# Performance work log

Hardware: AMD Instinct MI355X
Metric: run time of the kernel (lower is better)

Reference implementation:

```python
import jax, jax.numpy as jnp
import numpy as np

B, L, H = 8, 64, 128


def setup_inputs() -> dict:
    key = jax.random.key(0)
    ks = jax.random.split(key, 9)
    s = 1.0 / np.sqrt(H)

    def lin(k, shape):
        return jax.random.uniform(k, shape, jnp.float32, -s, s)

    return {
        "words_feats": jax.random.normal(ks[0], (B, L, H), jnp.float32),
        "words_masks": jnp.ones((B, L), jnp.int32),
        "Wl": lin(ks[1], (H, 1)), "bl": lin(ks[2], (1,)),
        "Wr": lin(ks[3], (H, 1)), "br": lin(ks[4], (1,)),
        "Wrep": lin(ks[5], (H, H)), "brep": lin(ks[6], (H,)),
        "Ws": lin(ks[7], (H, 1)), "bs": lin(ks[8], (1,)),
    }


def reference(words_feats, words_masks, Wl, bl, Wr, br, Wrep, brep, Ws, bs):
    # CYK chart DP. All sentences have full length L (masks all ones), so the
    # chart recursion runs L-1 levels with static trip count.
    Bsz, Ln, Hd = words_feats.shape
    ks_ = jnp.arange(Ln)  # split point k
    js_ = jnp.arange(Ln)  # start position j

    # chart T[b, i, j] = feature of span starting at j with length i+1
    T0 = jnp.zeros((Bsz, Ln, Ln, Hd), words_feats.dtype).at[:, 0].set(words_feats)

    def body(T, i):
        # left child:  T[b, k, j]            -> [B, k, j, H]
        left = T
        # right child: T[b, i-k-1, j+k+1]    -> [B, k, j, H] (clipped; masked below)
        rows = jnp.clip(i - ks_ - 1, 0, Ln - 1)                       # [k]
        cols = jnp.clip(js_[None, :] + ks_[:, None] + 1, 0, Ln - 1)   # [k, j]
        right = T[:, rows[:, None], cols]                             # [B, k, j, H]

        # 2-way attention combine of (left, right)
        sl = left @ Wl + bl                                            # [B, k, j, 1]
        sr = right @ Wr + br
        w = jax.nn.softmax(jnp.concatenate([sl, sr], axis=-1), axis=-1)
        h_hat = w[..., :1] * left + w[..., 1:] * right                 # [B, k, j, H]
        temp = jax.nn.relu(h_hat @ Wrep + brep) + h_hat

        # only k < i splits and spans with i + j < L exist; others are exact
        # zeros (matching the torch zero-initialized temp_h table)
        valid = (ks_[:, None] < i) & (js_[None, :] + i < Ln)           # [k, j]
        temp = jnp.where(valid[None, :, :, None], temp, 0.0)

        # softmax over ALL L split rows (zero rows contribute bias logits,
        # exactly as in the torch code)
        logits = (temp @ Ws + bs)[..., 0]                              # [B, k, j]
        split = jax.nn.softmax(logits, axis=1)                         # over k
        new_row = jnp.einsum('bkj,bkjh->bjh', split, temp)             # [B, j, H]
        new_row = jnp.where((js_ + i < Ln)[None, :, None], new_row, 0.0)
        return T.at[:, i].set(new_row), None

    T, _ = jax.lax.scan(body, T0, jnp.arange(1, Ln))
    return T[:, Ln - 1, 0]  # sentence feature: full span starting at 0
```

## Files before the change

kernel.cpp:

```cpp
#include <hip/hip_runtime.h>
#include <math.h>

#define Hd 128
#define Ln 64
#define Bsz 8
#define NBLK 256
#define NTHR 512
#define SLOTS 32


typedef __attribute__((ext_vector_type(8))) short short8v;
typedef __attribute__((ext_vector_type(4))) float f32x4;

__global__ void init_kernel(const float* __restrict__ wf, float* __restrict__ T,
                            int* __restrict__ flg) {
    int idx = blockIdx.x * 256 + threadIdx.x;
    int b = idx >> 13;
    int rest = idx & 8191;
    T[(size_t)b * (Ln * Ln * Hd) + rest] = wf[idx];
    if (idx < Bsz * Ln * Ln) flg[idx] = 0;
}

__device__ __forceinline__ float2 ld_row8(const float* p) {
    unsigned long long v = __hip_atomic_load((const unsigned long long*)p,
                                             __ATOMIC_RELAXED, __HIP_MEMORY_SCOPE_AGENT);
    return __builtin_bit_cast(float2, v);
}

__device__ __forceinline__ void wait_flag(const int* p) {
    while (__hip_atomic_load(p, __ATOMIC_RELAXED, __HIP_MEMORY_SCOPE_AGENT) == 0)
        __builtin_amdgcn_s_sleep(1);
    asm volatile("" ::: "memory");
}

__device__ __forceinline__ void bf_split3(float x, unsigned short& a0,
                                          unsigned short& a1, unsigned short& a2) {
    unsigned u0 = __builtin_bit_cast(unsigned, x);
    a0 = (unsigned short)(u0 >> 16);
    float f0 = __builtin_bit_cast(float, u0 & 0xffff0000u);
    float r1 = x - f0;
    unsigned u1 = __builtin_bit_cast(unsigned, r1);
    a1 = (unsigned short)(u1 >> 16);
    float f1 = __builtin_bit_cast(float, u1 & 0xffff0000u);
    float r2 = r1 - f1;
    a2 = (unsigned short)(__builtin_bit_cast(unsigned, r2) >> 16);
}

__device__ __forceinline__ float bfval(unsigned short v) {
    return __builtin_bit_cast(float, ((unsigned)v) << 16);
}

#define KSTEP(SK, B0, B1, B2)                                                   \
    {                                                                           \
        int off = ((16 * ch + (ln & 15)) << 7) +                                \
                  ((((SK << 2) + (ln >> 4)) ^ (ln & 15)) << 3);                 \
        short8v a0 = *(const short8v*)&sH0[off];                                \
        short8v a1 = *(const short8v*)&sH1[off];                                \
        short8v a2 = *(const short8v*)&sH2[off];                                \
        acc = __builtin_amdgcn_mfma_f32_16x16x32_bf16(a0, B0, acc, 0, 0, 0);    \
        acc = __builtin_amdgcn_mfma_f32_16x16x32_bf16(a0, B1, acc, 0, 0, 0);    \
        acc = __builtin_amdgcn_mfma_f32_16x16x32_bf16(a1, B0, acc, 0, 0, 0);    \
        acc = __builtin_amdgcn_mfma_f32_16x16x32_bf16(a0, B2, acc, 0, 0, 0);    \
        acc = __builtin_amdgcn_mfma_f32_16x16x32_bf16(a1, B1, acc, 0, 0, 0);    \
        acc = __builtin_amdgcn_mfma_f32_16x16x32_bf16(a2, B0, acc, 0, 0, 0);    \
    }

template<int NCH>
__device__ __forceinline__ void do_cell(
    int i, int jj, int b, int wv, int ln, int tid,
    const float* __restrict__ Tb, float* __restrict__ T, float* __restrict__ out,
    int* __restrict__ flgb,
    unsigned short* __restrict__ sH0, unsigned short* __restrict__ sH1,
    unsigned short* __restrict__ sH2,
    float (*part)[Ln], float* __restrict__ sER,
    const short8v (&B0)[4], const short8v (&B1)[4], const short8v (&B2)[4],
    float2 wlv, float2 wrv, float bl, float br, float bs, float wsc, float bbc)
{
    if (i >= 2) {
        wait_flag(&flgb[(i - 1) * Ln + jj]);
        wait_flag(&flgb[(i - 1) * Ln + jj + 1]);
    }

    float2 Lr[8], Rr[8];
    #pragma unroll
    for (int r = 0; r < 8; ++r) {
        int k = wv + 8 * r;
        int kcl = k < i ? k : i - 1;
        Lr[r] = ld_row8(Tb + ((size_t)kcl * Ln + jj) * Hd + 2 * ln);
        Rr[r] = ld_row8(Tb + ((size_t)(i - 1 - kcl) * Ln + (jj + kcl + 1)) * Hd + 2 * ln);
    }
    float pl[8], pr[8];
    #pragma unroll
    for (int r = 0; r < 8; ++r) {
        pl[r] = Lr[r].x * wlv.x + Lr[r].y * wlv.y;
        pr[r] = Rr[r].x * wrv.x + Rr[r].y * wrv.y;
    }
    #pragma unroll
    for (int off2 = 32; off2 > 0; off2 >>= 1) {
        #pragma unroll
        for (int r = 0; r < 8; ++r) {
            pl[r] += __shfl_xor(pl[r], off2);
            pr[r] += __shfl_xor(pr[r], off2);
        }
    }
    #pragma unroll
    for (int r = 0; r < 8; ++r) {
        int k = wv + 8 * r;
        float sl = pl[r] + bl, sr2 = pr[r] + br;
        float mm = fmaxf(sl, sr2);
        float e0 = __expf(sl - mm), e1 = __expf(sr2 - mm);
        float inv = 1.f / (e0 + e1);
        float w0 = e0 * inv, w1 = e1 * inv;
        float h0 = w0 * Lr[r].x + w1 * Rr[r].x;
        float h1 = w0 * Lr[r].y + w1 * Rr[r].y;
        unsigned short x0, x1, x2, y0, y1, y2;
        bf_split3(h0, x0, x1, x2);
        bf_split3(h1, y0, y1, y2);
        int off = (k << 7) + ((((ln >> 2)) ^ (k & 15)) << 3) + ((2 * ln) & 7);
        *(unsigned*)&sH0[off] = (unsigned)x0 | ((unsigned)y0 << 16);
        *(unsigned*)&sH1[off] = (unsigned)x1 | ((unsigned)y1 << 16);
        *(unsigned*)&sH2[off] = (unsigned)x2 | ((unsigned)y2 << 16);
    }
    __syncthreads();

    const int colc = 16 * wv + (ln & 15);
    float tmp[NCH][4];
    #pragma unroll
    for (int ch = 0; ch < NCH; ++ch) {
        f32x4 acc = {0.f, 0.f, 0.f, 0.f};
        KSTEP(0, B0[0], B1[0], B2[0])
        KSTEP(1, B0[1], B1[1], B2[1])
        KSTEP(2, B0[2], B1[2], B2[2])
        KSTEP(3, B0[3], B1[3], B2[3])
        float p[4];
        #pragma unroll
        for (int q = 0; q < 4; ++q) {
            int row = 16 * ch + (ln >> 4) * 4 + q;
            int offh = (row << 7) + (((colc >> 3) ^ (row & 15)) << 3) + (colc & 7);
            float h = (bfval(sH0[offh]) + bfval(sH1[offh])) + bfval(sH2[offh]);
            float t = fmaxf(acc[q] + bbc, 0.f) + h;
            tmp[ch][q] = t;
            p[q] = t * wsc;
        }
        #pragma unroll
        for (int off2 = 1; off2 <= 8; off2 <<= 1) {
            #pragma unroll
            for (int q = 0; q < 4; ++q) p[q] += __shfl_xor(p[q], off2);
        }
        if ((ln & 15) == 0) {
            #pragma unroll
            for (int q = 0; q < 4; ++q)
                part[wv][16 * ch + (ln >> 4) * 4 + q] = p[q];
        }
    }
    __syncthreads();

    if (wv == 0) {
        float lgv = -INFINITY;
        if (ln < i) {
            float ssum = part[0][ln];
            #pragma unroll
            for (int w = 1; w < 8; ++w) ssum += part[w][ln];
            lgv = ssum + bs;
        }
        float M = lgv;
        #pragma unroll
        for (int off2 = 32; off2 > 0; off2 >>= 1) M = fmaxf(M, __shfl_xor(M, off2));
        M = fmaxf(M, bs);
        float e = (ln < i) ? __expf(lgv - M) : 0.f;
        float S = e;
        #pragma unroll
        for (int off2 = 32; off2 > 0; off2 >>= 1) S += __shfl_xor(S, off2);
        sER[ln] = e;
        if (ln == 0) sER[64] = S + (float)(Ln - i) * __expf(bs - M);
    }
    __syncthreads();

    float v = 0.f;
    #pragma unroll
    for (int ch = 0; ch < NCH; ++ch) {
        #pragma unroll
        for (int q = 0; q < 4; ++q)
            v += sER[16 * ch + (ln >> 4) * 4 + q] * tmp[ch][q];
    }
    v += __shfl_xor(v, 16);
    v += __shfl_xor(v, 32);
    if (ln < 16) {
        float res = v / sER[64];
        __hip_atomic_store(&T[(((size_t)b * Ln + i) * Ln + jj) * Hd + colc], res,
                           __ATOMIC_RELAXED, __HIP_MEMORY_SCOPE_AGENT);
        if (i == Ln - 1) out[b * Hd + colc] = res;
    }
    __syncthreads();
    if (tid == 0)
        __hip_atomic_store(&flgb[i * Ln + jj], 1, __ATOMIC_RELAXED,
                           __HIP_MEMORY_SCOPE_AGENT);
}

__global__ __launch_bounds__(NTHR, 2)
void glt_df(const float* __restrict__ Wl, const float* __restrict__ blp,
            const float* __restrict__ Wr, const float* __restrict__ brp,
            const float* __restrict__ Wrep, const float* __restrict__ brepp,
            const float* __restrict__ Wsv, const float* __restrict__ bsp,
            float* __restrict__ T, int* __restrict__ flg, float* __restrict__ out)
{
    __shared__ __align__(16) unsigned short sH0[Ln * Hd];
    __shared__ __align__(16) unsigned short sH1[Ln * Hd];
    __shared__ __align__(16) unsigned short sH2[Ln * Hd];
    __shared__ float part[8][Ln];
    __shared__ float sER[68];

    const int tid = threadIdx.x;
    const int wv  = tid >> 6;
    const int ln  = tid & 63;
    const int b   = blockIdx.x & 7;
    const int s   = blockIdx.x >> 3;

    const int bcol = 16 * wv + (ln & 15);
    short8v B0[4], B1[4], B2[4];
    #pragma unroll
    for (int sk = 0; sk < 4; ++sk) {
        #pragma unroll
        for (int jx = 0; jx < 8; ++jx) {
            int k = 32 * sk + (ln >> 4) * 8 + jx;
            float w = Wrep[k * Hd + bcol];
            unsigned short w0, w1, w2;
            bf_split3(w, w0, w1, w2);
            B0[sk][jx] = (short)w0;
            B1[sk][jx] = (short)w1;
            B2[sk][jx] = (short)w2;
        }
    }

    const float bl = blp[0], br = brp[0], bs = bsp[0];
    const float2 wlv = *(const float2*)&Wl[2 * ln];
    const float2 wrv = *(const float2*)&Wr[2 * ln];
    const float wsc = Wsv[bcol];
    const float bbc = brepp[bcol];

    const float* Tb = T + (size_t)b * (Ln * Ln * Hd);
    int* flgb = flg + b * (Ln * Ln);

    int i = 1, jj = s;
    while (jj >= Ln - i) { jj -= Ln - i; ++i; }
    for (int t = 0; t < 63; ++t) {
        switch ((i + 15) >> 4) {
            case 1: do_cell<1>(i, jj, b, wv, ln, tid, Tb, T, out, flgb,
                               sH0, sH1, sH2, part, sER, B0, B1, B2,
                               wlv, wrv, bl, br, bs, wsc, bbc); break;
            case 2: do_cell<2>(i, jj, b, wv, ln, tid, Tb, T, out, flgb,
                               sH0, sH1, sH2, part, sER, B0, B1, B2,
                               wlv, wrv, bl, br, bs, wsc, bbc); break;
            case 3: do_cell<3>(i, jj, b, wv, ln, tid, Tb, T, out, flgb,
                               sH0, sH1, sH2, part, sER, B0, B1, B2,
                               wlv, wrv, bl, br, bs, wsc, bbc); break;
            default: do_cell<4>(i, jj, b, wv, ln, tid, Tb, T, out, flgb,
                                sH0, sH1, sH2, part, sER, B0, B1, B2,
                                wlv, wrv, bl, br, bs, wsc, bbc); break;
        }
        if (t < 62) {
            jj += SLOTS;
            while (jj >= Ln - i) { jj -= Ln - i; ++i; }
        }
    }
}

extern "C" void kernel_launch(void* const* d_in, const int* in_sizes, int n_in,
                              void* d_out, int out_size, void* d_ws, size_t ws_size,
                              hipStream_t stream)
{
    const float* wf   = (const float*)d_in[0];
    const float* Wl   = (const float*)d_in[2];
    const float* bl   = (const float*)d_in[3];
    const float* Wr   = (const float*)d_in[4];
    const float* br   = (const float*)d_in[5];
    const float* Wrep = (const float*)d_in[6];
    const float* brep = (const float*)d_in[7];
    const float* Ws   = (const float*)d_in[8];
    const float* bs   = (const float*)d_in[9];

    float* T   = (float*)d_ws;
    int*   flg = (int*)((char*)d_ws + (size_t)Bsz * Ln * Ln * Hd * 4);
    float* out = (float*)d_out;

    init_kernel<<<256, 256, 0, stream>>>(wf, T, flg);

    void* args[] = {(void*)&Wl, (void*)&bl, (void*)&Wr, (void*)&br,
                    (void*)&Wrep, (void*)&brep, (void*)&Ws, (void*)&bs,
                    (void*)&T, (void*)&flg, (void*)&out};
    hipLaunchCooperativeKernel((void*)glt_df, dim3(NBLK), dim3(NTHR),
                               args, 0, stream);
}
```

Measured before the change: 597.7 us.

## Speculatively compute middle splits early, finishing edge splits in fp32 after dependency

Each chart cell now waits only on row i-2 to compute the middle split points k=1..i-2 with MFMA. The two edge splits (k=0 and k=i-1), which depend on row i-1, are computed afterwards by waves 0 and 1 with an fp32 matvec against an LDS copy of Wrep, then merged into the split softmax. This shortens the per-level critical path of the inter-block dataflow wavefront. The cost is 64KB of extra LDS, which likely limits each CU to one block, plus some extra serial work on two waves.

Result: slower. 651.4 us (+9.0%).

```diff
diff --git a/kernel.cpp b/kernel.cpp
--- a/kernel.cpp
+++ b/kernel.cpp
@@ -50,20 +50,69 @@
     return __builtin_bit_cast(float, ((unsigned)v) << 16);
 }
 
-#define KSTEP(SK, B0, B1, B2)                                                   \
+#define KSTEP(SK, B0_, B1_, B2_)                                                \
     {                                                                           \
         int off = ((16 * ch + (ln & 15)) << 7) +                                \
                   ((((SK << 2) + (ln >> 4)) ^ (ln & 15)) << 3);                 \
         short8v a0 = *(const short8v*)&sH0[off];                                \
         short8v a1 = *(const short8v*)&sH1[off];                                \
         short8v a2 = *(const short8v*)&sH2[off];                                \
-        acc = __builtin_amdgcn_mfma_f32_16x16x32_bf16(a0, B0, acc, 0, 0, 0);    \
-        acc = __builtin_amdgcn_mfma_f32_16x16x32_bf16(a0, B1, acc, 0, 0, 0);    \
-        acc = __builtin_amdgcn_mfma_f32_16x16x32_bf16(a1, B0, acc, 0, 0, 0);    \
-        acc = __builtin_amdgcn_mfma_f32_16x16x32_bf16(a0, B2, acc, 0, 0, 0);    \
-        acc = __builtin_amdgcn_mfma_f32_16x16x32_bf16(a1, B1, acc, 0, 0, 0);    \
-        acc = __builtin_amdgcn_mfma_f32_16x16x32_bf16(a2, B0, acc, 0, 0, 0);    \
-    }
+        acc = __builtin_amdgcn_mfma_f32_16x16x32_bf16(a0, B0_, acc, 0, 0, 0);   \
+        acc = __builtin_amdgcn_mfma_f32_16x16x32_bf16(a0, B1_, acc, 0, 0, 0);   \
+        acc = __builtin_amdgcn_mfma_f32_16x16x32_bf16(a1, B0_, acc, 0, 0, 0);   \
+        acc = __builtin_amdgcn_mfma_f32_16x16x32_bf16(a0, B2_, acc, 0, 0, 0);   \
+        acc = __builtin_amdgcn_mfma_f32_16x16x32_bf16(a1, B1_, acc, 0, 0, 0);   \
+        acc = __builtin_amdgcn_mfma_f32_16x16x32_bf16(a2, B0_, acc, 0, 0, 0);   \
+    }
+
+__device__ __forceinline__ void final_row(
+    const float* __restrict__ lp, const float* __restrict__ rp,
+    const float* __restrict__ sW, float* __restrict__ sFh,
+    float* __restrict__ sFrow, float* __restrict__ sFin,
+    int ln, float2 wlv, float2 wrv, float bl, float br, float bs,
+    float wsA, float wsB, float bbA, float bbB)
+{
+    float2 L = ld_row8(lp + 2 * ln);
+    float2 R = ld_row8(rp + 2 * ln);
+    float pl = L.x * wlv.x + L.y * wlv.y;
+    float pr = R.x * wrv.x + R.y * wrv.y;
+    #pragma unroll
+    for (int off2 = 32; off2 > 0; off2 >>= 1) {
+        pl += __shfl_xor(pl, off2);
+        pr += __shfl_xor(pr, off2);
+    }
+    float sl = pl + bl, sr = pr + br;
+    float mm = fmaxf(sl, sr);
+    float e0 = __expf(sl - mm), e1 = __expf(sr - mm);
+    float inv = 1.f / (e0 + e1);
+    float w0 = e0 * inv, w1 = e1 * inv;
+    float2 hh;
+    hh.x = w0 * L.x + w1 * R.x;
+    hh.y = w0 * L.y + w1 * R.y;
+    *(float2*)&sFh[2 * ln] = hh;
+
+    const int c0 = ln, c1 = ln + 64;
+    const int x0 = ln & 31;
+    float a0 = 0.f, a1 = 0.f;
+    const float* sW0 = &sW[c0 * Hd];
+    const float* sW1 = &sW[c1 * Hd];
+    #pragma unroll 8
+    for (int hb = 0; hb < 32; ++hb) {
+        float4 w0v = *(const float4*)&sW0[(hb ^ x0) << 2];
+        float4 w1v = *(const float4*)&sW1[(hb ^ x0) << 2];
+        float4 hv = *(const float4*)&sFh[hb << 2];
+        a0 += hv.x * w0v.x + hv.y * w0v.y + hv.z * w0v.z + hv.w * w0v.w;
+        a1 += hv.x * w1v.x + hv.y * w1v.y + hv.z * w1v.z + hv.w * w1v.w;
+    }
+    float t0 = fmaxf(a0 + bbA, 0.f) + sFh[c0];
+    float t1 = fmaxf(a1 + bbB, 0.f) + sFh[c1];
+    sFrow[c0] = t0;
+    sFrow[c1] = t1;
+    float lg = t0 * wsA + t1 * wsB;
+    #pragma unroll
+    for (int off2 = 32; off2 > 0; off2 >>= 1) lg += __shfl_xor(lg, off2);
+    if (ln == 0) *sFin = lg + bs;
+}
 
 template<int NCH>
 __device__ __forceinline__ void do_cell(
@@ -72,92 +121,121 @@
     int* __restrict__ flgb,
     unsigned short* __restrict__ sH0, unsigned short* __restrict__ sH1,
     unsigned short* __restrict__ sH2,
+    const float* __restrict__ sW, float* __restrict__ sFh,
+    float* __restrict__ sF, float* __restrict__ sFin,
     float (*part)[Ln], float* __restrict__ sER,
     const short8v (&B0)[4], const short8v (&B1)[4], const short8v (&B2)[4],
-    float2 wlv, float2 wrv, float bl, float br, float bs, float wsc, float bbc)
+    float2 wlv, float2 wrv, float bl, float br, float bs,
+    float wsc, float bbc, float wsA, float wsB, float bbA, float bbB)
 {
-    if (i >= 2) {
-        wait_flag(&flgb[(i - 1) * Ln + jj]);
-        wait_flag(&flgb[(i - 1) * Ln + jj + 1]);
-    }
-
-    float2 Lr[8], Rr[8];
-    #pragma unroll
-    for (int r = 0; r < 8; ++r) {
-        int k = wv + 8 * r;
-        int kcl = k < i ? k : i - 1;
-        Lr[r] = ld_row8(Tb + ((size_t)kcl * Ln + jj) * Hd + 2 * ln);
-        Rr[r] = ld_row8(Tb + ((size_t)(i - 1 - kcl) * Ln + (jj + kcl + 1)) * Hd + 2 * ln);
-    }
-    float pl[8], pr[8];
-    #pragma unroll
-    for (int r = 0; r < 8; ++r) {
-        pl[r] = Lr[r].x * wlv.x + Lr[r].y * wlv.y;
-        pr[r] = Rr[r].x * wrv.x + Rr[r].y * wrv.y;
-    }
-    #pragma unroll
-    for (int off2 = 32; off2 > 0; off2 >>= 1) {
+    const bool spec = (i >= 3);
+
+    if (spec) {
+        wait_flag(&flgb[(i - 2) * Ln + jj]);
+        wait_flag(&flgb[(i - 2) * Ln + jj + 2]);
+
+        const int kmax = i - 2;
+        float2 Lr[8], Rr[8];
         #pragma unroll
         for (int r = 0; r < 8; ++r) {
-            pl[r] += __shfl_xor(pl[r], off2);
-            pr[r] += __shfl_xor(pr[r], off2);
-        }
-    }
-    #pragma unroll
-    for (int r = 0; r < 8; ++r) {
-        int k = wv + 8 * r;
-        float sl = pl[r] + bl, sr2 = pr[r] + br;
-        float mm = fmaxf(sl, sr2);
-        float e0 = __expf(sl - mm), e1 = __expf(sr2 - mm);
-        float inv = 1.f / (e0 + e1);
-        float w0 = e0 * inv, w1 = e1 * inv;
-        float h0 = w0 * Lr[r].x + w1 * Rr[r].x;
-        float h1 = w0 * Lr[r].y + w1 * Rr[r].y;
-        unsigned short x0, x1, x2, y0, y1, y2;
-        bf_split3(h0, x0, x1, x2);
-        bf_split3(h1, y0, y1, y2);
-        int off = (k << 7) + ((((ln >> 2)) ^ (k & 15)) << 3) + ((2 * ln) & 7);
-        *(unsigned*)&sH0[off] = (unsigned)x0 | ((unsigned)y0 << 16);
-        *(unsigned*)&sH1[off] = (unsigned)x1 | ((unsigned)y1 << 16);
-        *(unsigned*)&sH2[off] = (unsigned)x2 | ((unsigned)y2 << 16);
+            int k = wv + 8 * r;
+            int kcl = k < 1 ? 1 : (k > kmax ? kmax : k);
+            Lr[r] = ld_row8(Tb + ((size_t)kcl * Ln + jj) * Hd + 2 * ln);
+            Rr[r] = ld_row8(Tb + ((size_t)(i - 1 - kcl) * Ln + (jj + kcl + 1)) * Hd + 2 * ln);
+        }
+        float pl[8], pr[8];
+        #pragma unroll
+        for (int r = 0; r < 8; ++r) {
+            pl[r] = Lr[r].x * wlv.x + Lr[r].y * wlv.y;
+            pr[r] = Rr[r].x * wrv.x + Rr[r].y * wrv.y;
+        }
+        #pragma unroll
+        for (int off2 = 32; off2 > 0; off2 >>= 1) {
+            #pragma unroll
+            for (int r = 0; r < 8; ++r) {
+                pl[r] += __shfl_xor(pl[r], off2);
+                pr[r] += __shfl_xor(pr[r], off2);
+            }
+        }
+        #pragma unroll
+        for (int r = 0; r < 8; ++r) {
+            int k = wv + 8 * r;
+            float sl = pl[r] + bl, sr2 = pr[r] + br;
+            float mm = fmaxf(sl, sr2);
+            float e0 = __expf(sl - mm), e1 = __expf(sr2 - mm);
+            float inv = 1.f / (e0 + e1);
+            float w0 = e0 * inv, w1 = e1 * inv;
+            float h0 = w0 * Lr[r].x + w1 * Rr[r].x;
+            float h1 = w0 * Lr[r].y + w1 * Rr[r].y;
+            unsigned short x0s, x1s, x2s, y0s, y1s, y2s;
+            bf_split3(h0, x0s, x1s, x2s);
+            bf_split3(h1, y0s, y1s, y2s);
+            int off = (k << 7) + (((ln >> 2) ^ (k & 15)) << 3) + ((2 * ln) & 7);
+            *(unsigned*)&sH0[off] = (unsigned)x0s | ((unsigned)y0s << 16);
+            *(unsigned*)&sH1[off] = (unsigned)x1s | ((unsigned)y1s << 16);
+            *(unsigned*)&sH2[off] = (unsigned)x2s | ((unsigned)y2s << 16);
+        }
     }
     __syncthreads();
 
     const int colc = 16 * wv + (ln & 15);
     float tmp[NCH][4];
-    #pragma unroll
-    for (int ch = 0; ch < NCH; ++ch) {
-        f32x4 acc = {0.f, 0.f, 0.f, 0.f};
-        KSTEP(0, B0[0], B1[0], B2[0])
-        KSTEP(1, B0[1], B1[1], B2[1])
-        KSTEP(2, B0[2], B1[2], B2[2])
-        KSTEP(3, B0[3], B1[3], B2[3])
-        float p[4];
-        #pragma unroll
-        for (int q = 0; q < 4; ++q) {
-            int row = 16 * ch + (ln >> 4) * 4 + q;
-            int offh = (row << 7) + (((colc >> 3) ^ (row & 15)) << 3) + (colc & 7);
-            float h = (bfval(sH0[offh]) + bfval(sH1[offh])) + bfval(sH2[offh]);
-            float t = fmaxf(acc[q] + bbc, 0.f) + h;
-            tmp[ch][q] = t;
-            p[q] = t * wsc;
-        }
-        #pragma unroll
-        for (int off2 = 1; off2 <= 8; off2 <<= 1) {
+    if (spec) {
+        #pragma unroll
+        for (int ch = 0; ch < NCH; ++ch) {
+            f32x4 acc = {0.f, 0.f, 0.f, 0.f};
+            KSTEP(0, B0[0], B1[0], B2[0])
+            KSTEP(1, B0[1], B1[1], B2[1])
+            KSTEP(2, B0[2], B1[2], B2[2])
+            KSTEP(3, B0[3], B1[3], B2[3])
+            float p[4];
             #pragma unroll
-            for (int q = 0; q < 4; ++q) p[q] += __shfl_xor(p[q], off2);
-        }
-        if ((ln & 15) == 0) {
+            for (int q = 0; q < 4; ++q) {
+                int row = 16 * ch + (ln >> 4) * 4 + q;
+                int offh = (row << 7) + (((colc >> 3) ^ (row & 15)) << 3) + (colc & 7);
+                float h = (bfval(sH0[offh]) + bfval(sH1[offh])) + bfval(sH2[offh]);
+                float t = fmaxf(acc[q] + bbc, 0.f) + h;
+                tmp[ch][q] = t;
+                p[q] = t * wsc;
+            }
             #pragma unroll
-            for (int q = 0; q < 4; ++q)
-                part[wv][16 * ch + (ln >> 4) * 4 + q] = p[q];
-        }
+            for (int off2 = 1; off2 <= 8; off2 <<= 1) {
+                #pragma unroll
+                for (int q = 0; q < 4; ++q) p[q] += __shfl_xor(p[q], off2);
+            }
+            if ((ln & 15) == 0) {
+                #pragma unroll
+                for (int q = 0; q < 4; ++q)
+                    part[wv][16 * ch + (ln >> 4) * 4 + q] = p[q];
+            }
+        }
+    } else {
+        #pragma unroll
+        for (int ch = 0; ch < NCH; ++ch)
+            #pragma unroll
+            for (int q = 0; q < 4; ++q) tmp[ch][q] = 0.f;
+    }
+
+    if (wv == 0) {
+        if (i >= 2) wait_flag(&flgb[(i - 1) * Ln + jj + 1]);
+        final_row(Tb + (size_t)jj * Hd,
+                  Tb + ((size_t)(i - 1) * Ln + (jj + 1)) * Hd,
+                  sW, sFh, sF, &sFin[0], ln,
+                  wlv, wrv, bl, br, bs, wsA, wsB, bbA, bbB);
+    } else if (wv == 1 && i >= 2) {
+        wait_flag(&flgb[(i - 1) * Ln + jj]);
+        final_row(Tb + ((size_t)(i - 1) * Ln + jj) * Hd,
+                  Tb + (size_t)(jj + i) * Hd,
+                  sW, sFh + Hd, sF + Hd, &sFin[1], ln,
+                  wlv, wrv, bl, br, bs, wsA, wsB, bbA, bbB);
     }
     __syncthreads();
 
     if (wv == 0) {
         float lgv = -INFINITY;
-        if (ln < i) {
+        if (ln == 0) lgv = sFin[0];
+        else if (ln == i - 1) lgv = sFin[1];
+        else if (ln <= i - 2) {
             float ssum = part[0][ln];
             #pragma unroll
             for (int w = 1; w < 8; ++w) ssum += part[w][ln];
@@ -171,8 +249,14 @@
         float S = e;
         #pragma unroll
         for (int off2 = 32; off2 > 0; off2 >>= 1) S += __shfl_xor(S, off2);
-        sER[ln] = e;
-        if (ln == 0) sER[64] = S + (float)(Ln - i) * __expf(bs - M);
+        float espec = (ln >= 1 && ln <= i - 2) ? e : 0.f;
+        sER[ln] = espec;
+        if (ln == 0) {
+            sER[64] = S + (float)(Ln - i) * __expf(bs - M);
+            sER[65] = e;
+            if (i == 1) sER[66] = 0.f;
+        }
+        if (ln == i - 1 && i >= 2) sER[66] = e;
     }
     __syncthreads();
 
@@ -185,6 +269,7 @@
     }
     v += __shfl_xor(v, 16);
     v += __shfl_xor(v, 32);
+    v += sER[65] * sF[colc] + sER[66] * sF[Hd + colc];
     if (ln < 16) {
         float res = v / sER[64];
         __hip_atomic_store(&T[(((size_t)b * Ln + i) * Ln + jj) * Hd + colc], res,
@@ -204,9 +289,13 @@
             const float* __restrict__ Wsv, const float* __restrict__ bsp,
             float* __restrict__ T, int* __restrict__ flg, float* __restrict__ out)
 {
+    __shared__ __align__(16) float sW[Hd * Hd];
     __shared__ __align__(16) unsigned short sH0[Ln * Hd];
     __shared__ __align__(16) unsigned short sH1[Ln * Hd];
     __shared__ __align__(16) unsigned short sH2[Ln * Hd];
+    __shared__ __align__(16) float sFh[2 * Hd];
+    __shared__ __align__(16) float sF[2 * Hd];
+    __shared__ float sFin[2];
     __shared__ float part[8][Ln];
     __shared__ float sER[68];
 
@@ -215,6 +304,20 @@
     const int ln  = tid & 63;
     const int b   = blockIdx.x & 7;
     const int s   = blockIdx.x >> 3;
+
+    #pragma unroll
+    for (int it = 0; it < 8; ++it) {
+        int idx4 = tid + it * NTHR;
+        int h  = idx4 & 127;
+        int c4 = (idx4 >> 7) << 2;
+        float4 v = *(const float4*)&Wrep[h * Hd + c4];
+        float vv[4] = {v.x, v.y, v.z, v.w};
+        #pragma unroll
+        for (int q = 0; q < 4; ++q) {
+            int c = c4 + q;
+            sW[c * Hd + ((((h >> 2) ^ (c & 31)) << 2) | (h & 3))] = vv[q];
+        }
+    }
 
     const int bcol = 16 * wv + (ln & 15);
     short8v B0[4], B1[4], B2[4];
@@ -235,8 +338,9 @@
     const float bl = blp[0], br = brp[0], bs = bsp[0];
     const float2 wlv = *(const float2*)&Wl[2 * ln];
     const float2 wrv = *(const float2*)&Wr[2 * ln];
-    const float wsc = Wsv[bcol];
-    const float bbc = brepp[bcol];
+    const float wsc = Wsv[bcol], bbc = brepp[bcol];
+    const float wsA = Wsv[ln], wsB = Wsv[ln + 64];
+    const float bbA = brepp[ln], bbB = brepp[ln + 64];
 
     const float* Tb = T + (size_t)b * (Ln * Ln * Hd);
     int* flgb = flg + b * (Ln * Ln);
@@ -244,19 +348,24 @@
     int i = 1, jj = s;
     while (jj >= Ln - i) { jj -= Ln - i; ++i; }
     for (int t = 0; t < 63; ++t) {
-        switch ((i + 15) >> 4) {
+        int nch = (i < 3) ? 1 : ((i + 14) >> 4);
+        switch (nch) {
             case 1: do_cell<1>(i, jj, b, wv, ln, tid, Tb, T, out, flgb,
-                               sH0, sH1, sH2, part, sER, B0, B1, B2,
-                               wlv, wrv, bl, br, bs, wsc, bbc); break;
+                               sH0, sH1, sH2, sW, sFh, sF, sFin, part, sER,
+                               B0, B1, B2, wlv, wrv, bl, br, bs,
+                               wsc, bbc, wsA, wsB, bbA, bbB); break;
             case 2: do_cell<2>(i, jj, b, wv, ln, tid, Tb, T, out, flgb,
-                               sH0, sH1, sH2, part, sER, B0, B1, B2,
-                               wlv, wrv, bl, br, bs, wsc, bbc); break;
+                               sH0, sH1, sH2, sW, sFh, sF, sFin, part, sER,
+                               B0, B1, B2, wlv, wrv, bl, br, bs,
+                               wsc, bbc, wsA, wsB, bbA, bbB); break;
             case 3: do_cell<3>(i, jj, b, wv, ln, tid, Tb, T, out, flgb,
-                               sH0, sH1, sH2, part, sER, B0, B1, B2,
-                               wlv, wrv, bl, br, bs, wsc, bbc); break;
+                               sH0, sH1, sH2, sW, sFh, sF, sFin, part, sER,
+                               B0, B1, B2, wlv, wrv, bl, br, bs,
+                               wsc, bbc, wsA, wsB, bbA, bbB); break;
             default: do_cell<4>(i, jj, b, wv, ln, tid, Tb, T, out, flgb,
-                                sH0, sH1, sH2, part, sER, B0, B1, B2,
-                                wlv, wrv, bl, br, bs, wsc, bbc); break;
+                                sH0, sH1, sH2, sW, sFh, sF, sFin, part, sER,
+                                B0, B1, B2, wlv, wrv, bl, br, bs,
+                                wsc, bbc, wsA, wsB, bbA, bbB); break;
         }
         if (t < 62) {
             jj += SLOTS;
```
